# Kernel optimization log

Hardware: AMD Instinct MI355X
Metric: run time of the kernel (lower is better)

## Reference

```python
import jax, jax.numpy as jnp
import numpy as np
from jax import lax

N = 65536   # number of nodes
D = 1024    # in_feat_dim
K = 32      # hhr_number


def setup_inputs() -> dict:
    key = jax.random.key(0)
    k1, k2 = jax.random.split(key)
    node_feat = jax.random.normal(k1, (N, D), dtype=jnp.float32)
    # mapping_vectors: hhr_number vectors of length in_feat_dim (torch stores (d,1); we use (K, d))
    V = jax.random.normal(k2, (K, D), dtype=jnp.float32)
    return {"node_feat": node_feat, "V": V}


def reference(node_feat, V):
    # Each layer: h = h @ (I - v v^T / (v^T v))
    # Algebraically identical rank-1 form: h - (h @ v) v^T / (v^T v)
    def step(h, v):
        vv = jnp.dot(v, v)                       # scalar v^T v
        hv = h @ v                               # [N]
        h = h - jnp.outer(hv, v) / vv            # [N, D] rank-1 update
        return h, None

    h, _ = lax.scan(step, node_feat, V)
    return h
```

## Files before the change

kernel.cpp:

```cpp
#include <hip/hip_runtime.h>

#define DD 1024
#define KK 32

__global__ void vv_inv_kernel(const float* __restrict__ V, float* __restrict__ vvinv) {
    int k = blockIdx.x;
    const float* v = V + k * DD;
    int t = threadIdx.x;
    float s = 0.f;
    for (int i = t; i < DD; i += 256) { float x = v[i]; s += x * x; }
    #pragma unroll
    for (int off = 32; off >= 1; off >>= 1) s += __shfl_xor(s, off, 64);
    __shared__ float red[4];
    if ((t & 63) == 0) red[t >> 6] = s;
    __syncthreads();
    if (t == 0) vvinv[k] = 1.0f / (red[0] + red[1] + red[2] + red[3]);
}

__global__ __launch_bounds__(1024) void hh_tower_kernel(
    const float* __restrict__ H, const float* __restrict__ V,
    const float* __restrict__ vvinv, float* __restrict__ out, int Nn)
{
    extern __shared__ float Vl[];
    {
        const float4* src = (const float4*)V;
        float4* dst = (float4*)Vl;
        int t = threadIdx.x;
        #pragma unroll
        for (int i = 0; i < 8; ++i) dst[t + (i << 10)] = src[t + (i << 10)];
    }
    __syncthreads();

    const int lane = threadIdx.x & 63;
    const int wid  = threadIdx.x >> 6;
    const int gwave  = blockIdx.x * (blockDim.x >> 6) + wid;
    const int nwaves = gridDim.x * (blockDim.x >> 6);

    const int s  = (lane >> 2) & 1;
    const int o0 = (lane << 3) + (s << 2);
    const int o1 = (lane << 3) + ((1 - s) << 2);
    const int o2 = 512 + o0;
    const int o3 = 512 + o1;

    const int ngroups = Nn >> 2;
    for (int g = gwave; g < ngroups; g += nwaves) {
        const int base = g << 2;
        float4 h0[4], h1[4], h2[4], h3[4];
        #pragma unroll
        for (int m = 0; m < 4; ++m) {
            const float* row = H + (size_t)(base + m) * DD;
            h0[m] = *(const float4*)(row + o0);
            h1[m] = *(const float4*)(row + o1);
            h2[m] = *(const float4*)(row + o2);
            h3[m] = *(const float4*)(row + o3);
        }

        #pragma unroll 2
        for (int k = 0; k < KK; ++k) {
            const float* vr = Vl + (k << 10);
            const float4 v0 = *(const float4*)(vr + o0);
            const float4 v1 = *(const float4*)(vr + o1);
            const float4 v2 = *(const float4*)(vr + o2);
            const float4 v3 = *(const float4*)(vr + o3);
            const float vi = vvinv[k];

            float dot[4];
            #pragma unroll
            for (int m = 0; m < 4; ++m) {
                float pa = h0[m].x * v0.x + h0[m].y * v0.y + h0[m].z * v0.z + h0[m].w * v0.w;
                float pb = h1[m].x * v1.x + h1[m].y * v1.y + h1[m].z * v1.z + h1[m].w * v1.w;
                float pc = h2[m].x * v2.x + h2[m].y * v2.y + h2[m].z * v2.z + h2[m].w * v2.w;
                float pd = h3[m].x * v3.x + h3[m].y * v3.y + h3[m].z * v3.z + h3[m].w * v3.w;
                dot[m] = (pa + pb) + (pc + pd);
            }
            #pragma unroll
            for (int off = 1; off <= 32; off <<= 1) {
                #pragma unroll
                for (int m = 0; m < 4; ++m) dot[m] += __shfl_xor(dot[m], off, 64);
            }
            #pragma unroll
            for (int m = 0; m < 4; ++m) {
                const float gc = dot[m] * vi;
                h0[m].x -= gc * v0.x; h0[m].y -= gc * v0.y; h0[m].z -= gc * v0.z; h0[m].w -= gc * v0.w;
                h1[m].x -= gc * v1.x; h1[m].y -= gc * v1.y; h1[m].z -= gc * v1.z; h1[m].w -= gc * v1.w;
                h2[m].x -= gc * v2.x; h2[m].y -= gc * v2.y; h2[m].z -= gc * v2.z; h2[m].w -= gc * v2.w;
                h3[m].x -= gc * v3.x; h3[m].y -= gc * v3.y; h3[m].z -= gc * v3.z; h3[m].w -= gc * v3.w;
            }
        }

        #pragma unroll
        for (int m = 0; m < 4; ++m) {
            float* row = out + (size_t)(base + m) * DD;
            *(float4*)(row + o0) = h0[m];
            *(float4*)(row + o1) = h1[m];
            *(float4*)(row + o2) = h2[m];
            *(float4*)(row + o3) = h3[m];
        }
    }
}

extern "C" void kernel_launch(void* const* d_in, const int* in_sizes, int n_in,
                              void* d_out, int out_size, void* d_ws, size_t ws_size,
                              hipStream_t stream) {
    const float* H = (const float*)d_in[0];
    const float* V = (const float*)d_in[1];
    float* vvinv = (float*)d_ws;
    float* out = (float*)d_out;
    int Nn = in_sizes[0] / DD;

    vv_inv_kernel<<<KK, 256, 0, stream>>>(V, vvinv);

    const int smem = KK * DD * (int)sizeof(float);
    hipFuncSetAttribute((const void*)hh_tower_kernel,
                        hipFuncAttributeMaxDynamicSharedMemorySize, smem);
    hh_tower_kernel<<<256, 1024, smem, stream>>>(H, V, vvinv, out, Nn);
}
```

Measured before the change: 553.2 us.

## Compose the Householder chain into a WY-style dot-then-update over H

This replaces the sequential chain of 32 rank-1 projections with a composed form. First the Gram matrix of V is built and triangularly inverted into a small 32x32 mixing matrix. Then one pass computes all 32 dot products H·v_k per row, and a second pass applies H - (U M) V using wave-uniform scalar loads of V. This removes the per-layer cross-lane shuffle reductions and their serial dependency. In exchange H is read twice, the partial dots are combined with global atomics, and the path only runs when the workspace can hold the N×32 dot buffer. The reordered arithmetic can also change rounding relative to the sequential reference.

Measured after the change: 1.175 ms. 112% more time.

```diff
diff --git a/kernel.cpp b/kernel.cpp
--- a/kernel.cpp
+++ b/kernel.cpp
@@ -2,6 +2,134 @@
 
 #define DD 1024
 #define KK 32
+
+
+__global__ void gram_kernel(const float* __restrict__ V, float* __restrict__ S) {
+    const int i = blockIdx.x, j = blockIdx.y;
+    const int t = threadIdx.x;
+    const float4* vi = (const float4*)(V + i * DD);
+    const float4* vj = (const float4*)(V + j * DD);
+    float s = 0.f;
+    #pragma unroll
+    for (int q = 0; q < 4; ++q) {
+        float4 a = vi[t + (q << 6)];
+        float4 b = vj[t + (q << 6)];
+        s += a.x * b.x + a.y * b.y + a.z * b.z + a.w * b.w;
+    }
+    #pragma unroll
+    for (int off = 32; off >= 1; off >>= 1) s += __shfl_xor(s, off, 64);
+    if (t == 0) S[i * KK + j] = s;
+}
+
+__global__ void compose_kernel(const float* __restrict__ S, float* __restrict__ Mt) {
+    const int r = threadIdx.x;
+    float C[KK];
+    #pragma unroll
+    for (int j = 0; j < KK; ++j) {
+        float acc = (r == j) ? 1.f : 0.f;
+        #pragma unroll
+        for (int i = 0; i < j; ++i) {
+            float coef = S[i * KK + j] / S[i * KK + i];
+            acc -= coef * C[i];
+        }
+        C[j] = acc;
+        if (r < KK) Mt[j * KK + r] = acc / S[j * KK + j];
+    }
+}
+
+__global__ __launch_bounds__(256, 4) void dots_kernel(
+    const float* __restrict__ H, const float* __restrict__ V,
+    float* __restrict__ U) {
+    const int lane = threadIdx.x & 63;
+    const int wid  = threadIdx.x >> 6;
+    const int gw   = (blockIdx.x << 2) + wid;
+    const int ng   = gw >> 2;
+    const int q    = __builtin_amdgcn_readfirstlane(gw & 3);
+    const int n    = (ng << 6) + lane;
+
+    const float* hrow = H + (size_t)n * DD + (q << 8);
+    float u[KK];
+    #pragma unroll
+    for (int k = 0; k < KK; ++k) u[k] = 0.f;
+
+    for (int c = 0; c < 8; ++c) {
+        const int dbase = c << 5;
+        float4 h4[8];
+        #pragma unroll
+        for (int x = 0; x < 8; ++x) h4[x] = *(const float4*)(hrow + dbase + (x << 2));
+        const float* vb = V + (q << 8) + dbase;
+        #pragma unroll
+        for (int k = 0; k < KK; ++k) {
+            const float* vk = vb + k * DD;
+            #pragma unroll
+            for (int x = 0; x < 8; ++x) {
+                u[k] = fmaf(h4[x].x, vk[(x << 2) + 0], u[k]);
+                u[k] = fmaf(h4[x].y, vk[(x << 2) + 1], u[k]);
+                u[k] = fmaf(h4[x].z, vk[(x << 2) + 2], u[k]);
+                u[k] = fmaf(h4[x].w, vk[(x << 2) + 3], u[k]);
+            }
+        }
+    }
+    float* up = U + ((size_t)n << 5);
+    #pragma unroll
+    for (int k = 0; k < KK; ++k) atomicAdd(up + k, u[k]);
+}
+
+__global__ __launch_bounds__(256, 4) void update_kernel(
+    const float* __restrict__ H, const float* __restrict__ V,
+    const float* __restrict__ U, const float* __restrict__ Mt,
+    float* __restrict__ out) {
+    const int lane = threadIdx.x & 63;
+    const int wid  = threadIdx.x >> 6;
+    const int gw   = (blockIdx.x << 2) + wid;
+    const int ng   = gw >> 2;
+    const int q    = __builtin_amdgcn_readfirstlane(gw & 3);
+    const int n    = (ng << 6) + lane;
+
+    float uu[KK];
+    {
+        const float4* up = (const float4*)(U + ((size_t)n << 5));
+        #pragma unroll
+        for (int x = 0; x < 8; ++x) {
+            float4 t4 = up[x];
+            uu[(x << 2) + 0] = t4.x; uu[(x << 2) + 1] = t4.y;
+            uu[(x << 2) + 2] = t4.z; uu[(x << 2) + 3] = t4.w;
+        }
+    }
+    float g[KK];
+    #pragma unroll
+    for (int j = 0; j < KK; ++j) {
+        const float* mr = Mt + j * KK;
+        float a = 0.f;
+        #pragma unroll
+        for (int i = 0; i < KK; ++i) a = fmaf(uu[i], mr[i], a);
+        g[j] = a;
+    }
+
+    const float* hrow = H + (size_t)n * DD + (q << 8);
+    float*       orow = out + (size_t)n * DD + (q << 8);
+    for (int c = 0; c < 8; ++c) {
+        const int dbase = c << 5;
+        float4 h4[8];
+        #pragma unroll
+        for (int x = 0; x < 8; ++x) h4[x] = *(const float4*)(hrow + dbase + (x << 2));
+        const float* vb = V + (q << 8) + dbase;
+        #pragma unroll
+        for (int j = 0; j < KK; ++j) {
+            const float* vj = vb + j * DD;
+            const float gj = g[j];
+            #pragma unroll
+            for (int x = 0; x < 8; ++x) {
+                h4[x].x = fmaf(-gj, vj[(x << 2) + 0], h4[x].x);
+                h4[x].y = fmaf(-gj, vj[(x << 2) + 1], h4[x].y);
+                h4[x].z = fmaf(-gj, vj[(x << 2) + 2], h4[x].z);
+                h4[x].w = fmaf(-gj, vj[(x << 2) + 3], h4[x].w);
+            }
+        }
+        #pragma unroll
+        for (int x = 0; x < 8; ++x) *(float4*)(orow + dbase + (x << 2)) = h4[x];
+    }
+}
 
 __global__ void vv_inv_kernel(const float* __restrict__ V, float* __restrict__ vvinv) {
     int k = blockIdx.x;
@@ -30,18 +158,15 @@
         for (int i = 0; i < 8; ++i) dst[t + (i << 10)] = src[t + (i << 10)];
     }
     __syncthreads();
-
     const int lane = threadIdx.x & 63;
     const int wid  = threadIdx.x >> 6;
     const int gwave  = blockIdx.x * (blockDim.x >> 6) + wid;
     const int nwaves = gridDim.x * (blockDim.x >> 6);
-
     const int s  = (lane >> 2) & 1;
     const int o0 = (lane << 3) + (s << 2);
     const int o1 = (lane << 3) + ((1 - s) << 2);
     const int o2 = 512 + o0;
     const int o3 = 512 + o1;
-
     const int ngroups = Nn >> 2;
     for (int g = gwave; g < ngroups; g += nwaves) {
         const int base = g << 2;
@@ -54,7 +179,6 @@
             h2[m] = *(const float4*)(row + o2);
             h3[m] = *(const float4*)(row + o3);
         }
-
         #pragma unroll 2
         for (int k = 0; k < KK; ++k) {
             const float* vr = Vl + (k << 10);
@@ -63,7 +187,6 @@
             const float4 v2 = *(const float4*)(vr + o2);
             const float4 v3 = *(const float4*)(vr + o3);
             const float vi = vvinv[k];
-
             float dot[4];
             #pragma unroll
             for (int m = 0; m < 4; ++m) {
@@ -87,7 +210,6 @@
                 h3[m].x -= gc * v3.x; h3[m].y -= gc * v3.y; h3[m].z -= gc * v3.z; h3[m].w -= gc * v3.w;
             }
         }
-
         #pragma unroll
         for (int m = 0; m < 4; ++m) {
             float* row = out + (size_t)(base + m) * DD;
@@ -104,14 +226,29 @@
                               hipStream_t stream) {
     const float* H = (const float*)d_in[0];
     const float* V = (const float*)d_in[1];
-    float* vvinv = (float*)d_ws;
     float* out = (float*)d_out;
-    int Nn = in_sizes[0] / DD;
-
-    vv_inv_kernel<<<KK, 256, 0, stream>>>(V, vvinv);
-
-    const int smem = KK * DD * (int)sizeof(float);
-    hipFuncSetAttribute((const void*)hh_tower_kernel,
-                        hipFuncAttributeMaxDynamicSharedMemorySize, smem);
-    hh_tower_kernel<<<256, 1024, smem, stream>>>(H, V, vvinv, out, Nn);
-}
+    const int Nn = in_sizes[0] / DD;
+
+    const size_t U_bytes  = (size_t)Nn * KK * sizeof(float);
+    const size_t need     = U_bytes + 2 * KK * KK * sizeof(float);
+
+    if (ws_size >= need) {
+        float* U  = (float*)d_ws;
+        float* S  = (float*)((char*)d_ws + U_bytes);
+        float* Mt = S + KK * KK;
+
+        hipMemsetAsync(U, 0, U_bytes, stream);
+        gram_kernel<<<dim3(KK, KK), 64, 0, stream>>>(V, S);
+        compose_kernel<<<1, 64, 0, stream>>>(S, Mt);
+        const int nblocks = Nn >> 6;
+        dots_kernel<<<nblocks, 256, 0, stream>>>(H, V, U);
+        update_kernel<<<nblocks, 256, 0, stream>>>(H, V, U, Mt, out);
+    } else {
+        float* vvinv = (float*)d_ws;
+        vv_inv_kernel<<<KK, 256, 0, stream>>>(V, vvinv);
+        const int smem = KK * DD * (int)sizeof(float);
+        hipFuncSetAttribute((const void*)hh_tower_kernel,
+                            hipFuncAttributeMaxDynamicSharedMemorySize, smem);
+        hh_tower_kernel<<<256, 1024, smem, stream>>>(H, V, vvinv, out, Nn);
+    }
+}
```
